# Kernel optimization log

Hardware: AMD Instinct MI355X
Metric: run time of the kernel (lower is better)

## Reference

```python
import jax, jax.numpy as jnp
import numpy as np

EPS = 1e-5

def _ln(x, g, b):
    mu = jnp.mean(x, axis=-1, keepdims=True)
    var = jnp.mean((x - mu) ** 2, axis=-1, keepdims=True)
    return (x - mu) * jax.lax.rsqrt(var + EPS) * g + b

def _lin(x, W, b):
    return x @ W + b

def setup_inputs() -> dict:
    B, D_IN, H = 32768, 512, 512
    key = jax.random.key(0)
    ks = jax.random.split(key, 20)
    def W(k, din, dout):
        return jax.random.normal(k, (din, dout), jnp.float32) / np.sqrt(din)
    inp = {
        'x': jax.random.normal(ks[0], (B, D_IN), jnp.float32),
        'h_prev': jax.random.normal(ks[1], (B, H), jnp.float32),
        's_prev': jax.random.normal(ks[2], (B, H), jnp.float32),
        'W_in': W(ks[3], D_IN, H), 'b_in': jnp.zeros((H,), jnp.float32),
        'g_ln_in': jnp.ones((H,), jnp.float32), 'b_ln_in': jnp.zeros((H,), jnp.float32),
        'g_ln_r': jnp.ones((H,), jnp.float32), 'b_ln_r': jnp.zeros((H,), jnp.float32),
        'g_ln_z': jnp.ones((H,), jnp.float32), 'b_ln_z': jnp.zeros((H,), jnp.float32),
        'g_ln_h': jnp.ones((H,), jnp.float32), 'b_ln_h': jnp.zeros((H,), jnp.float32),
        'W_r': W(ks[4], H, H), 'b_r': jnp.zeros((H,), jnp.float32),
        'W_z': W(ks[5], H, H), 'b_z': jnp.zeros((H,), jnp.float32),
        'W_k': W(ks[6], H, H), 'b_k': jnp.zeros((H,), jnp.float32),
        'W_v': W(ks[7], H, H), 'b_v': jnp.zeros((H,), jnp.float32),
        'W_h': W(ks[8], H, H), 'b_h': jnp.zeros((H,), jnp.float32),
        'W_d': W(ks[9], H, H), 'b_d': jnp.zeros((H,), jnp.float32),
    }
    return inp

def reference(x, h_prev, s_prev, W_in, b_in, g_ln_in, b_ln_in,
              g_ln_r, b_ln_r, g_ln_z, b_ln_z, g_ln_h, b_ln_h,
              W_r, b_r, W_z, b_z, W_k, b_k, W_v, b_v, W_h, b_h, W_d, b_d):
    # u = LN(input_proj(x))
    u = _ln(_lin(x, W_in, b_in), g_ln_in, b_ln_in)
    r = jax.nn.sigmoid(_ln(_lin(u, W_r, b_r), g_ln_r, b_ln_r))  # computed as in original (unused downstream)
    z = jax.nn.sigmoid(_ln(_lin(u, W_z, b_z), g_ln_z, b_ln_z))
    k = _lin(u, W_k, b_k)
    v = _lin(u, W_v, b_v)
    decay = jax.nn.sigmoid(_lin(u, W_d, b_d))
    s = decay * s_prev + k * v
    c = jnp.tanh(_ln(_lin(u + s, W_h, b_h), g_ln_h, b_ln_h))
    h = (1.0 - z) * c + z * h_prev
    return (h, s)
```

## Files before the change

kernel.cpp:

```cpp
#include <hip/hip_runtime.h>

typedef __attribute__((ext_vector_type(8))) short bf16x8;
typedef __attribute__((ext_vector_type(4))) float f32x4;

#define LN_EPS 1e-5f
#define MSZ ((size_t)32768 * 512)
#define WSZ ((size_t)512 * 512)

typedef const __attribute__((address_space(1))) void* gptr_t;
typedef __attribute__((address_space(3))) void* lptr_t;

__device__ __forceinline__ float b2f(unsigned short h) {
    unsigned int u = ((unsigned int)h) << 16;
    return __uint_as_float(u);
}
__device__ __forceinline__ short f2b(float f) {
    unsigned int u = __float_as_uint(f);
    unsigned int r = (u + 0x7FFFu + ((u >> 16) & 1u)) >> 16;
    return (short)(unsigned short)r;
}
__device__ __forceinline__ float sigmoid_f(float x) {
    return 1.0f / (1.0f + __expf(-x));
}
__device__ __forceinline__ float ldS(const void* p, size_t i, int isbf) {
    return isbf ? b2f(((const unsigned short*)p)[i]) : ((const float*)p)[i];
}
__device__ __forceinline__ void ld8(const void* p, size_t i, int isbf, float* o) {
    if (isbf) {
        bf16x8 v = *(const bf16x8*)((const unsigned short*)p + i);
        #pragma unroll
        for (int j = 0; j < 8; ++j) o[j] = b2f((unsigned short)v[j]);
    } else {
        f32x4 a = *(const f32x4*)((const float*)p + i);
        f32x4 b = *(const f32x4*)((const float*)p + i + 4);
        #pragma unroll
        for (int j = 0; j < 4; ++j) { o[j] = a[j]; o[4 + j] = b[j]; }
    }
}

__global__ void detect_dtype(const unsigned int* __restrict__ ones, int* __restrict__ flag) {
    if (threadIdx.x == 0 && blockIdx.x == 0)
        *flag = (ones[0] == 0x3F803F80u) ? 1 : 0;
}

__global__ __launch_bounds__(256) void transpose6(
    const void* __restrict__ s0, const void* __restrict__ s1,
    const void* __restrict__ s2, const void* __restrict__ s3,
    const void* __restrict__ s4, const void* __restrict__ s5,
    unsigned short* __restrict__ d0, unsigned short* __restrict__ d1,
    unsigned short* __restrict__ d2, unsigned short* __restrict__ d3,
    unsigned short* __restrict__ d4, unsigned short* __restrict__ d5,
    const int* __restrict__ flagp)
{
    const int isbf = *flagp;
    const void* srcs[6] = {s0, s1, s2, s3, s4, s5};
    unsigned short* dsts[6] = {d0, d1, d2, d3, d4, d5};
    const void* src = srcs[blockIdx.z];
    unsigned short* dst = dsts[blockIdx.z];

    __shared__ unsigned short tile[32][33];
    int tx = threadIdx.x, ty = threadIdx.y;
    int colbase = blockIdx.x * 32;
    int rowbase = blockIdx.y * 32;
    #pragma unroll
    for (int i = 0; i < 32; i += 8)
        tile[ty + i][tx] = (unsigned short)f2b(
            ldS(src, (size_t)(rowbase + ty + i) * 512 + colbase + tx, isbf));
    __syncthreads();
    #pragma unroll
    for (int i = 0; i < 32; i += 8)
        dst[(size_t)(colbase + ty + i) * 512 + rowbase + tx] = tile[tx][ty + i];
}

__global__ __launch_bounds__(256) void cvt_x(
    const float* __restrict__ x, unsigned short* __restrict__ Xb,
    const int* __restrict__ flagp)
{
    if (*flagp) return;
    size_t i = ((size_t)blockIdx.x * 256 + threadIdx.x) * 8;
    f32x4 a = *(const f32x4*)&x[i];
    f32x4 b = *(const f32x4*)&x[i + 4];
    bf16x8 o;
    #pragma unroll
    for (int j = 0; j < 4; ++j) { o[j] = f2b(a[j]); o[4 + j] = f2b(b[j]); }
    *(bf16x8*)&Xb[i] = o;
}

__global__ __launch_bounds__(256) void gemm_bt(
    const void* __restrict__ Araw, const unsigned short* __restrict__ Aconv,
    const unsigned short* __restrict__ BT,
    const void* __restrict__ b0, const void* __restrict__ b1,
    const void* __restrict__ b2, const void* __restrict__ b3,
    unsigned short* __restrict__ C0, unsigned short* __restrict__ C1,
    unsigned short* __restrict__ C2, unsigned short* __restrict__ C3,
    int nbshift, const int* __restrict__ flagp)
{
    const int isbf = *flagp;
    const int K = 512;
    __shared__ unsigned short smem[128 * 136];
    unsigned short* As = smem;
    unsigned short* Bs = smem + 128 * 64;

    const unsigned short* Ab = isbf ? (const unsigned short*)Araw : Aconv;

    int t = threadIdx.x;
    int lane = t & 63;
    int wave = t >> 6;
    int wm = (wave >> 1) * 64;
    int wn = (wave & 1) * 64;

    int bflat = blockIdx.x;
    int xcd = bflat & 7;
    int bi = bflat >> 3;
    int n0 = (bi & ((1 << nbshift) - 1)) << 7;
    int mi = bi >> nbshift;
    int m0 = ((xcd << 5) + mi) << 7;

    int lr = lane >> 3;
    int lg = lane & 7;
    int gsrc = lg ^ lr;

    size_t a_off[4], b_off[4];
    #pragma unroll
    for (int i = 0; i < 4; ++i) {
        int c = wave * 4 + i;
        a_off[i] = (size_t)(m0 + 8 * c + lr) * K + gsrc * 8;
        b_off[i] = (size_t)(n0 + 8 * c + lr) * K + gsrc * 8;
    }

    int ml = lane & 15;
    int kg = lane >> 4;
    int sw = ml & 7;

    f32x4 acc[4][4] = {};

    for (int k0 = 0; k0 < K; k0 += 64) {
        #pragma unroll
        for (int i = 0; i < 4; ++i) {
            int c = wave * 4 + i;
            __builtin_amdgcn_global_load_lds(
                (gptr_t)(const void*)(Ab + a_off[i] + k0),
                (lptr_t)(void*)(As + c * 512), 16, 0, 0);
        }
        #pragma unroll
        for (int i = 0; i < 4; ++i) {
            int c = wave * 4 + i;
            __builtin_amdgcn_global_load_lds(
                (gptr_t)(const void*)(BT + b_off[i] + k0),
                (lptr_t)(void*)(Bs + c * 512), 16, 0, 0);
        }
        __syncthreads();

        #pragma unroll
        for (int ks = 0; ks < 2; ++ks) {
            bf16x8 af[4], bfr[4];
            #pragma unroll
            for (int i = 0; i < 4; ++i) {
                int ga = ((ks << 2) + kg) ^ sw;
                af[i]  = *(const bf16x8*)&As[(wm + i * 16 + ml) * 64 + ga * 8];
                bfr[i] = *(const bf16x8*)&Bs[(wn + i * 16 + ml) * 64 + ga * 8];
            }
            #pragma unroll
            for (int i = 0; i < 4; ++i)
                #pragma unroll
                for (int j = 0; j < 4; ++j)
                    acc[i][j] = __builtin_amdgcn_mfma_f32_16x16x32_bf16(
                        af[i], bfr[j], acc[i][j], 0, 0, 0);
        }
        __syncthreads();
    }

    int seg = n0 >> 9;
    const void* bias = (seg == 0) ? b0 : (seg == 1) ? b1 : (seg == 2) ? b2 : b3;
    unsigned short* Cs = (seg == 0) ? C0 : (seg == 1) ? C1 : (seg == 2) ? C2 : C3;
    int ncol0 = n0 & 511;
    int cq = lane >> 4;
    int cl = lane & 15;
    #pragma unroll
    for (int j = 0; j < 4; ++j) {
        float bv = ldS(bias, ncol0 + wn + j * 16 + cl, isbf);
        #pragma unroll
        for (int i = 0; i < 4; ++i) {
            #pragma unroll
            for (int r = 0; r < 4; ++r) {
                smem[(wm + i * 16 + cq * 4 + r) * 136 + wn + j * 16 + cl] =
                    (unsigned short)f2b(acc[i][j][r] + bv);
            }
        }
    }
    __syncthreads();

    int tr = t >> 4;
    int tc = (t & 15) * 8;
    #pragma unroll
    for (int it = 0; it < 8; ++it) {
        int rl = it * 16 + tr;
        size_t idx = (size_t)(m0 + rl) * 512 + ncol0 + tc;
        *(bf16x8*)&Cs[idx] = *(bf16x8*)&smem[rl * 136 + tc];
    }
}

__global__ __launch_bounds__(256) void fused_sa(
    const unsigned short* __restrict__ klin,
    const unsigned short* __restrict__ vlin,
    const unsigned short* __restrict__ dlin,
    const unsigned short* __restrict__ u,
    const void* __restrict__ s_prev,
    void* __restrict__ dout,
    const int* __restrict__ flagp)
{
    const int isbf = *flagp;
    size_t i = ((size_t)blockIdx.x * 256 + threadIdx.x) * 8;
    bf16x8 k8 = *(const bf16x8*)&klin[i];
    bf16x8 v8 = *(const bf16x8*)&vlin[i];
    bf16x8 d8 = *(const bf16x8*)&dlin[i];
    bf16x8 u8 = *(const bf16x8*)&u[i];
    float sp[8];
    ld8(s_prev, i, isbf, sp);

    float sv[8];
    bf16x8 a8;
    #pragma unroll
    for (int z = 0; z < 8; ++z) {
        float dv = sigmoid_f(b2f((unsigned short)d8[z]));
        sv[z] = dv * sp[z] + b2f((unsigned short)k8[z]) * b2f((unsigned short)v8[z]);
        a8[z] = f2b(b2f((unsigned short)u8[z]) + sv[z]);
    }
    if (isbf) {
        bf16x8 s8;
        #pragma unroll
        for (int z = 0; z < 8; ++z) s8[z] = f2b(sv[z]);
        *(bf16x8*)&((unsigned short*)dout)[MSZ + i] = s8;
    } else {
        f32x4 lo, hi;
        #pragma unroll
        for (int z = 0; z < 4; ++z) { lo[z] = sv[z]; hi[z] = sv[4 + z]; }
        *(f32x4*)&((float*)dout)[MSZ + i] = lo;
        *(f32x4*)&((float*)dout)[MSZ + i + 4] = hi;
    }
    *(bf16x8*)&((unsigned short*)dout)[i] = a8;
}

__global__ __launch_bounds__(256) void ln_rows(
    const unsigned short* __restrict__ X,
    const void* __restrict__ g,
    const void* __restrict__ b,
    unsigned short* __restrict__ Y,
    const int* __restrict__ flagp)
{
    const int isbf = *flagp;
    int wave = threadIdx.x >> 6, lane = threadIdx.x & 63;
    size_t row = (size_t)blockIdx.x * 4 + wave;
    size_t base = row * 512 + (size_t)lane * 8;

    bf16x8 xv = *(const bf16x8*)&X[base];
    float x[8];
    float s = 0.f, s2 = 0.f;
    #pragma unroll
    for (int i = 0; i < 8; ++i) {
        x[i] = b2f((unsigned short)xv[i]);
        s += x[i]; s2 += x[i] * x[i];
    }
    #pragma unroll
    for (int off = 32; off > 0; off >>= 1) {
        s  += __shfl_xor(s, off);
        s2 += __shfl_xor(s2, off);
    }
    float mu = s * (1.f / 512.f);
    float var = s2 * (1.f / 512.f) - mu * mu;
    float rs = rsqrtf(var + LN_EPS);

    float gv[8], bv[8];
    ld8(g, (size_t)lane * 8, isbf, gv);
    ld8(b, (size_t)lane * 8, isbf, bv);
    bf16x8 o;
    #pragma unroll
    for (int i = 0; i < 8; ++i)
        o[i] = f2b((x[i] - mu) * rs * gv[i] + bv[i]);
    *(bf16x8*)&Y[base] = o;
}

__global__ __launch_bounds__(256) void fused_out(
    const unsigned short* __restrict__ hlin,
    const unsigned short* __restrict__ zlin,
    const void* __restrict__ h_prev,
    const void* __restrict__ g_z, const void* __restrict__ b_z,
    const void* __restrict__ g_h, const void* __restrict__ b_h,
    void* __restrict__ dout,
    const int* __restrict__ flagp)
{
    const int isbf = *flagp;
    int wave = threadIdx.x >> 6, lane = threadIdx.x & 63;
    size_t row = (size_t)blockIdx.x * 4 + wave;
    size_t base = row * 512 + (size_t)lane * 8;

    bf16x8 zv8 = *(const bf16x8*)&zlin[base];
    bf16x8 hv8 = *(const bf16x8*)&hlin[base];
    float zf[8], hf[8];
    float sz = 0.f, sz2 = 0.f, sh = 0.f, sh2 = 0.f;
    #pragma unroll
    for (int i = 0; i < 8; ++i) {
        zf[i] = b2f((unsigned short)zv8[i]);
        hf[i] = b2f((unsigned short)hv8[i]);
        sz += zf[i]; sz2 += zf[i] * zf[i];
        sh += hf[i]; sh2 += hf[i] * hf[i];
    }
    #pragma unroll
    for (int off = 32; off > 0; off >>= 1) {
        sz  += __shfl_xor(sz, off);  sz2 += __shfl_xor(sz2, off);
        sh  += __shfl_xor(sh, off);  sh2 += __shfl_xor(sh2, off);
    }
    float muz = sz * (1.f / 512.f);
    float rsz = rsqrtf(sz2 * (1.f / 512.f) - muz * muz + LN_EPS);
    float muh = sh * (1.f / 512.f);
    float rsh = rsqrtf(sh2 * (1.f / 512.f) - muh * muh + LN_EPS);

    float gz[8], bz[8], gh[8], bh[8], hp[8];
    ld8(g_z, (size_t)lane * 8, isbf, gz);
    ld8(b_z, (size_t)lane * 8, isbf, bz);
    ld8(g_h, (size_t)lane * 8, isbf, gh);
    ld8(b_h, (size_t)lane * 8, isbf, bh);
    ld8(h_prev, base, isbf, hp);

    float hout[8];
    #pragma unroll
    for (int i = 0; i < 8; ++i) {
        float z = sigmoid_f((zf[i] - muz) * rsz * gz[i] + bz[i]);
        float c = tanhf((hf[i] - muh) * rsh * gh[i] + bh[i]);
        hout[i] = (1.f - z) * c + z * hp[i];
    }
    if (isbf) {
        bf16x8 o;
        #pragma unroll
        for (int i = 0; i < 8; ++i) o[i] = f2b(hout[i]);
        *(bf16x8*)&((unsigned short*)dout)[base] = o;
    } else {
        f32x4 a, b;
        #pragma unroll
        for (int i = 0; i < 4; ++i) { a[i] = hout[i]; b[i] = hout[4 + i]; }
        *(f32x4*)&((float*)dout)[base] = a;
        *(f32x4*)&((float*)dout)[base + 4] = b;
    }
}

extern "C" void kernel_launch(void* const* d_in, const int* in_sizes, int n_in,
                              void* d_out, int out_size, void* d_ws, size_t ws_size,
                              hipStream_t stream)
{
    (void)in_sizes; (void)n_in; (void)out_size; (void)ws_size;

    const void* x       = d_in[0];
    const void* h_prev  = d_in[1];
    const void* s_prev  = d_in[2];
    const void* W_in    = d_in[3];
    const void* b_in    = d_in[4];
    const void* g_ln_in = d_in[5];
    const void* b_ln_in = d_in[6];
    const void* g_ln_z  = d_in[9];
    const void* b_ln_z  = d_in[10];
    const void* g_ln_h  = d_in[11];
    const void* b_ln_h  = d_in[12];
    const void* W_z     = d_in[15];
    const void* b_z     = d_in[16];
    const void* W_k     = d_in[17];
    const void* b_k     = d_in[18];
    const void* W_v     = d_in[19];
    const void* b_v     = d_in[20];
    const void* W_h     = d_in[21];
    const void* b_h     = d_in[22];
    const void* W_d     = d_in[23];
    const void* b_d     = d_in[24];

    unsigned short* ws = (unsigned short*)d_ws;
    unsigned short* U  = ws;
    unsigned short* L  = ws + MSZ;
    unsigned short* Kb = ws + 2 * MSZ;
    unsigned short* Vb = ws + 3 * MSZ;
    unsigned short* Db = ws + 4 * MSZ;
    unsigned short* WT = ws + 5 * MSZ;
    unsigned short* WT_in = WT;
    unsigned short* WT_z  = WT + 1 * WSZ;
    unsigned short* WT_k  = WT + 2 * WSZ;
    unsigned short* WT_v  = WT + 3 * WSZ;
    unsigned short* WT_d  = WT + 4 * WSZ;
    unsigned short* WT_h  = WT + 5 * WSZ;
    int* flag = (int*)(WT + 6 * WSZ);

    detect_dtype<<<1, 64, 0, stream>>>((const unsigned int*)g_ln_in, flag);
    transpose6<<<dim3(16, 16, 6), dim3(32, 8), 0, stream>>>(
        W_in, W_z, W_k, W_v, W_d, W_h,
        WT_in, WT_z, WT_k, WT_v, WT_d, WT_h, flag);

    cvt_x<<<8192, 256, 0, stream>>>((const float*)x, Vb, flag);

    gemm_bt<<<1024, 256, 0, stream>>>(x, Vb, WT_in,
                                      b_in, b_in, b_in, b_in,
                                      L, L, L, L, 2, flag);
    ln_rows<<<8192, 256, 0, stream>>>(L, g_ln_in, b_ln_in, U, flag);

    gemm_bt<<<4096, 256, 0, stream>>>(U, U, WT_z,
                                      b_z, b_k, b_v, b_d,
                                      L, Kb, Vb, Db, 4, flag);

    fused_sa<<<8192, 256, 0, stream>>>(Kb, Vb, Db, U, s_prev, d_out, flag);

    gemm_bt<<<1024, 256, 0, stream>>>(d_out, (const unsigned short*)d_out, WT_h,
                                      b_h, b_h, b_h, b_h,
                                      Kb, Kb, Kb, Kb, 2, flag);

    fused_out<<<8192, 256, 0, stream>>>(Kb, L, h_prev,
                                        g_ln_z, b_ln_z, g_ln_h, b_ln_h,
                                        d_out, flag);
}
```

Measured before the change: 524.2 us.

## Fuse fp32-to-bf16 conversion of x into input GEMM and use BM=64 tiles

Removes the standalone cvt_x kernel. The first GEMM now loads fp32 x directly, converts it to bf16 in registers and writes the swizzled tile into LDS itself. The GEMM is templated on the M tile size, and the two N=512 GEMMs (input projection and W_h) now use 64-row tiles with twice as many blocks, to fill more of the CUs. The cost is that the converted A loads go through registers instead of async global_load_lds, and the smaller tiles reuse B less.

```diff
diff --git a/kernel.cpp b/kernel.cpp
--- a/kernel.cpp
+++ b/kernel.cpp
@@ -72,20 +72,7 @@
         dst[(size_t)(colbase + ty + i) * 512 + rowbase + tx] = tile[tx][ty + i];
 }
 
-__global__ __launch_bounds__(256) void cvt_x(
-    const float* __restrict__ x, unsigned short* __restrict__ Xb,
-    const int* __restrict__ flagp)
-{
-    if (*flagp) return;
-    size_t i = ((size_t)blockIdx.x * 256 + threadIdx.x) * 8;
-    f32x4 a = *(const f32x4*)&x[i];
-    f32x4 b = *(const f32x4*)&x[i + 4];
-    bf16x8 o;
-    #pragma unroll
-    for (int j = 0; j < 4; ++j) { o[j] = f2b(a[j]); o[4 + j] = f2b(b[j]); }
-    *(bf16x8*)&Xb[i] = o;
-}
-
+template<int BM, bool CONV>
 __global__ __launch_bounds__(256) void gemm_bt(
     const void* __restrict__ Araw, const unsigned short* __restrict__ Aconv,
     const unsigned short* __restrict__ BT,
@@ -97,16 +84,20 @@
 {
     const int isbf = *flagp;
     const int K = 512;
-    __shared__ unsigned short smem[128 * 136];
+    constexpr int AI = BM / 32;
+    constexpr int SMEM_STG = BM * 64 + 128 * 64;
+    constexpr int SMEM_EPI = BM * 136;
+    constexpr int SMEMN = SMEM_STG > SMEM_EPI ? SMEM_STG : SMEM_EPI;
+    __shared__ unsigned short smem[SMEMN];
     unsigned short* As = smem;
-    unsigned short* Bs = smem + 128 * 64;
+    unsigned short* Bs = smem + BM * 64;
 
     const unsigned short* Ab = isbf ? (const unsigned short*)Araw : Aconv;
 
     int t = threadIdx.x;
     int lane = t & 63;
     int wave = t >> 6;
-    int wm = (wave >> 1) * 64;
+    int wm = (wave >> 1) * (BM / 2);
     int wn = (wave & 1) * 64;
 
     int bflat = blockIdx.x;
@@ -114,33 +105,60 @@
     int bi = bflat >> 3;
     int n0 = (bi & ((1 << nbshift) - 1)) << 7;
     int mi = bi >> nbshift;
-    int m0 = ((xcd << 5) + mi) << 7;
+    constexpr int MTX = (32768 / BM) / 8;
+    int m0 = (xcd * MTX + mi) * BM;
 
     int lr = lane >> 3;
     int lg = lane & 7;
     int gsrc = lg ^ lr;
 
-    size_t a_off[4], b_off[4];
+    size_t a_off[AI], b_off[4];
+    #pragma unroll
+    for (int i = 0; i < AI; ++i) {
+        int c = wave * AI + i;
+        a_off[i] = (size_t)(m0 + 8 * c + lr) * K + gsrc * 8;
+    }
     #pragma unroll
     for (int i = 0; i < 4; ++i) {
         int c = wave * 4 + i;
-        a_off[i] = (size_t)(m0 + 8 * c + lr) * K + gsrc * 8;
         b_off[i] = (size_t)(n0 + 8 * c + lr) * K + gsrc * 8;
     }
+
+    constexpr int TPR = 256 / BM;
+    constexpr int NG = 8 / TPR;
+    int cr = t / TPR;
+    int cg0 = (t % TPR) * NG;
 
     int ml = lane & 15;
     int kg = lane >> 4;
     int sw = ml & 7;
 
-    f32x4 acc[4][4] = {};
+    f32x4 acc[AI][4] = {};
+
+    const bool conv_now = CONV && !isbf;
 
     for (int k0 = 0; k0 < K; k0 += 64) {
-        #pragma unroll
-        for (int i = 0; i < 4; ++i) {
-            int c = wave * 4 + i;
-            __builtin_amdgcn_global_load_lds(
-                (gptr_t)(const void*)(Ab + a_off[i] + k0),
-                (lptr_t)(void*)(As + c * 512), 16, 0, 0);
+        if (conv_now) {
+            const float* Af = (const float*)Araw;
+            #pragma unroll
+            for (int j = 0; j < NG; ++j) {
+                int G = cg0 + j;
+                size_t gi = (size_t)(m0 + cr) * K + k0 + G * 8;
+                f32x4 lo = *(const f32x4*)&Af[gi];
+                f32x4 hi = *(const f32x4*)&Af[gi + 4];
+                bf16x8 p;
+                #pragma unroll
+                for (int z = 0; z < 4; ++z) { p[z] = f2b(lo[z]); p[4 + z] = f2b(hi[z]); }
+                *(bf16x8*)&As[cr * 64 + ((G ^ (cr & 7)) * 8)] = p;
+            }
+        } else {
+            #pragma unroll
+            for (int i = 0; i < AI; ++i) {
+                int c = wave * AI + i;
+                __builtin_amdgcn_global_load_lds(
+                    (gptr_t)(const void*)(Ab + a_off[i] + k0),
+                    (lptr_t)(void*)(As + c * 512), 16, 0, 0);
+            }
         }
         #pragma unroll
         for (int i = 0; i < 4; ++i) {
@@ -153,15 +171,19 @@
 
         #pragma unroll
         for (int ks = 0; ks < 2; ++ks) {
-            bf16x8 af[4], bfr[4];
+            bf16x8 af[AI], bfr[4];
+            #pragma unroll
+            for (int i = 0; i < AI; ++i) {
+                int ga = ((ks << 2) + kg) ^ sw;
+                af[i] = *(const bf16x8*)&As[(wm + i * 16 + ml) * 64 + ga * 8];
+            }
             #pragma unroll
             for (int i = 0; i < 4; ++i) {
                 int ga = ((ks << 2) + kg) ^ sw;
-                af[i]  = *(const bf16x8*)&As[(wm + i * 16 + ml) * 64 + ga * 8];
                 bfr[i] = *(const bf16x8*)&Bs[(wn + i * 16 + ml) * 64 + ga * 8];
             }
             #pragma unroll
-            for (int i = 0; i < 4; ++i)
+            for (int i = 0; i < AI; ++i)
                 #pragma unroll
                 for (int j = 0; j < 4; ++j)
                     acc[i][j] = __builtin_amdgcn_mfma_f32_16x16x32_bf16(
@@ -180,7 +202,7 @@
     for (int j = 0; j < 4; ++j) {
         float bv = ldS(bias, ncol0 + wn + j * 16 + cl, isbf);
         #pragma unroll
-        for (int i = 0; i < 4; ++i) {
+        for (int i = 0; i < AI; ++i) {
             #pragma unroll
             for (int r = 0; r < 4; ++r) {
                 smem[(wm + i * 16 + cq * 4 + r) * 136 + wn + j * 16 + cl] =
@@ -193,7 +215,7 @@
     int tr = t >> 4;
     int tc = (t & 15) * 8;
     #pragma unroll
-    for (int it = 0; it < 8; ++it) {
+    for (int it = 0; it < BM / 16; ++it) {
         int rl = it * 16 + tr;
         size_t idx = (size_t)(m0 + rl) * 512 + ncol0 + tc;
         *(bf16x8*)&Cs[idx] = *(bf16x8*)&smem[rl * 136 + tc];
@@ -391,22 +413,24 @@
         W_in, W_z, W_k, W_v, W_d, W_h,
         WT_in, WT_z, WT_k, WT_v, WT_d, WT_h, flag);
 
-    cvt_x<<<8192, 256, 0, stream>>>((const float*)x, Vb, flag);
-
-    gemm_bt<<<1024, 256, 0, stream>>>(x, Vb, WT_in,
-                                      b_in, b_in, b_in, b_in,
-                                      L, L, L, L, 2, flag);
+    gemm_bt<64, true><<<2048, 256, 0, stream>>>(
+        x, (const unsigned short*)x, WT_in,
+        b_in, b_in, b_in, b_in,
+        L, L, L, L, 2, flag);
+
     ln_rows<<<8192, 256, 0, stream>>>(L, g_ln_in, b_ln_in, U, flag);
 
-    gemm_bt<<<4096, 256, 0, stream>>>(U, U, WT_z,
-                                      b_z, b_k, b_v, b_d,
-                                      L, Kb, Vb, Db, 4, flag);
+    gemm_bt<128, false><<<4096, 256, 0, stream>>>(
+        U, U, WT_z,
+        b_z, b_k, b_v, b_d,
+        L, Kb, Vb, Db, 4, flag);
 
     fused_sa<<<8192, 256, 0, stream>>>(Kb, Vb, Db, U, s_prev, d_out, flag);
 
-    gemm_bt<<<1024, 256, 0, stream>>>(d_out, (const unsigned short*)d_out, WT_h,
-                                      b_h, b_h, b_h, b_h,
-                                      Kb, Kb, Kb, Kb, 2, flag);
+    gemm_bt<64, false><<<2048, 256, 0, stream>>>(
+        d_out, (const unsigned short*)d_out, WT_h,
+        b_h, b_h, b_h, b_h,
+        Kb, Kb, Kb, Kb, 2, flag);
 
     fused_out<<<8192, 256, 0, stream>>>(Kb, L, h_prev,
                                         g_ln_z, b_ln_z, g_ln_h, b_ln_h,
```

Result: no change. 523.5 us (-0.1%).
